# Kernel tuning notes

Hardware: AMD Instinct MI355X
Metric: run time of the kernel (lower is better)

## Reference

```python
import jax, jax.numpy as jnp
import numpy as np

B, H, S, D = 4, 16, 2048, 64

def setup_inputs() -> dict:
    key = jax.random.key(0)
    kq, kk, kv, km = jax.random.split(key, 4)
    q = jax.random.normal(kq, (B, H, S, D), dtype=jnp.float32)
    k = jax.random.normal(kk, (B, H, S, D), dtype=jnp.float32)
    v = jax.random.normal(kv, (B, H, S, D), dtype=jnp.float32)
    mask = jax.random.randint(km, (B, H, S, S), 0, 2, dtype=jnp.int32)
    return {"q": q, "k": k, "v": v, "mask": mask}

def reference(q, k, v, mask):
    d_k = q.shape[-1]
    scale = 1.0 / jnp.sqrt(jnp.asarray(d_k, dtype=q.dtype))
    # scores: [B, H, Sq, Sk]
    scores = jnp.einsum('bhqd,bhkd->bhqk', q, k) * scale
    scores = jnp.where(mask == 0, jnp.asarray(-10000.0, dtype=scores.dtype), scores)
    attn = jax.nn.softmax(scores, axis=-1)
    out = jnp.einsum('bhqk,bhkd->bhqd', attn, v)
    return (out, attn)
```

## Files before the change

### kernel.cpp

```cpp
#include <hip/hip_runtime.h>
#include <hip/hip_bf16.h>

typedef short bf16x8 __attribute__((ext_vector_type(8)));
typedef float f32x4 __attribute__((ext_vector_type(4)));
typedef unsigned short u16x8 __attribute__((ext_vector_type(8)));

#define DEVI static __device__ __forceinline__

constexpr int Bb = 4, Hh = 16, Ss = 2048, Dd = 64;
constexpr int BH = Bb * Hh;
constexpr float SCALE = 0.125f;
constexpr long QKV_ELEMS = (long)BH * Ss * Dd;
constexpr long MASK_ELEMS = (long)BH * Ss * Ss;

DEVI unsigned short f2bf(float f) {
  __hip_bfloat16 h = __float2bfloat16(f);
  unsigned short u;
  __builtin_memcpy(&u, &h, 2);
  return u;
}
DEVI float bflo(unsigned int u) { unsigned int x = u << 16;        float f; __builtin_memcpy(&f, &x, 4); return f; }
DEVI float bfhi(unsigned int u) { unsigned int x = u & 0xffff0000u; float f; __builtin_memcpy(&f, &x, 4); return f; }

DEVI int pidx(int q, int k) { return (q << 12) + ((k << 1) ^ ((q & 7) << 4)); }

DEVI bf16x8 cvt8(const float* p) {
  float4 a = *reinterpret_cast<const float4*>(p);
  float4 b = *reinterpret_cast<const float4*>(p + 4);
  bf16x8 r;
  r[0] = (short)f2bf(a.x); r[1] = (short)f2bf(a.y); r[2] = (short)f2bf(a.z); r[3] = (short)f2bf(a.w);
  r[4] = (short)f2bf(b.x); r[5] = (short)f2bf(b.y); r[6] = (short)f2bf(b.z); r[7] = (short)f2bf(b.w);
  return r;
}

__global__ __launch_bounds__(256) void bitpack(const int* __restrict__ mask,
                                               unsigned long long* __restrict__ bits)
{
  const long wid = (((long)blockIdx.x * 256 + threadIdx.x) >> 6);
  const int lane = threadIdx.x & 63;
  const long NW = ((long)gridDim.x * 256) >> 6;
  for (long W = wid; W < (MASK_ELEMS >> 8); W += NW) {
    const int* p = mask + (W << 8) + lane;
    const unsigned long long b0 = __ballot(__builtin_nontemporal_load(p) != 0);
    const unsigned long long b1 = __ballot(__builtin_nontemporal_load(p + 64) != 0);
    const unsigned long long b2 = __ballot(__builtin_nontemporal_load(p + 128) != 0);
    const unsigned long long b3 = __ballot(__builtin_nontemporal_load(p + 192) != 0);
    if (lane == 0) {
      ulonglong4 o; o.x = b0; o.y = b1; o.z = b2; o.w = b3;
      *reinterpret_cast<ulonglong4*>(bits + (W << 2)) = o;
    }
  }
}

__global__ __launch_bounds__(256) void cvt_qk(const float* __restrict__ q, const float* __restrict__ k,
                                              unsigned short* __restrict__ qb, unsigned short* __restrict__ kb)
{
  const long i = ((long)blockIdx.x * 256 + threadIdx.x) * 4;
  if (i >= QKV_ELEMS) return;
  const float4 a = *reinterpret_cast<const float4*>(q + i);
  ushort4 oa; oa.x = f2bf(a.x); oa.y = f2bf(a.y); oa.z = f2bf(a.z); oa.w = f2bf(a.w);
  *reinterpret_cast<ushort4*>(qb + i) = oa;
  const float4 b = *reinterpret_cast<const float4*>(k + i);
  ushort4 ob; ob.x = f2bf(b.x); ob.y = f2bf(b.y); ob.z = f2bf(b.z); ob.w = f2bf(b.w);
  *reinterpret_cast<ushort4*>(kb + i) = ob;
}

__global__ __launch_bounds__(256) void cvt_vt(const float* __restrict__ v, unsigned short* __restrict__ vt)
{
  __shared__ float tile[64][65];
  const int bh = blockIdx.x >> 5;
  const int s0 = (blockIdx.x & 31) << 6;
  const int t  = threadIdx.x;
  {
    const int c = (t & 15) << 2;
    const float* src = v + ((long)bh * Ss + s0) * Dd;
    for (int rr = (t >> 4); rr < 64; rr += 16) {
      const float4 a = *reinterpret_cast<const float4*>(src + rr * Dd + c);
      tile[rr][c] = a.x; tile[rr][c + 1] = a.y; tile[rr][c + 2] = a.z; tile[rr][c + 3] = a.w;
    }
  }
  __syncthreads();
  {
    const int d  = t >> 2;
    const int sc = (t & 3) << 4;
    unsigned short* dst = vt + ((long)bh * Dd + d) * Ss + s0 + sc;
    u16x8 v0, v1;
#pragma unroll
    for (int j = 0; j < 8; ++j) v0[j] = f2bf(tile[sc + j][d]);
#pragma unroll
    for (int j = 0; j < 8; ++j) v1[j] = f2bf(tile[sc + 8 + j][d]);
    *reinterpret_cast<u16x8*>(dst)     = v0;
    *reinterpret_cast<u16x8*>(dst + 8) = v1;
  }
}

template<bool PRE>
__global__ __launch_bounds__(256, 2)
void attn_main(const float* __restrict__ qf, const float* __restrict__ kf,
               const float* __restrict__ vf, const int* __restrict__ mask,
               const unsigned short* __restrict__ qb,
               const unsigned short* __restrict__ kbp,
               const unsigned short* __restrict__ vt,
               const unsigned long long* __restrict__ bits,
               float* __restrict__ out, float* __restrict__ attn)
{
  __shared__ __align__(16) char Pb[16 * 2048 * 2];
  __shared__ float rpart[4][16];
  __shared__ float rinv[16];

  const int tid  = threadIdx.x;
  const int wave = tid >> 6;
  const int lane = tid & 63;
  const int l15  = lane & 15;
  const int lg   = lane >> 4;

  const int bh    = blockIdx.x >> 7;
  const int qbase = (blockIdx.x & 127) << 4;

  bf16x8 qfrag0, qfrag1;
  {
    const long qrow = (long)(bh * Ss + qbase + l15) * Dd + lg * 8;
    if (PRE) {
      qfrag0 = *reinterpret_cast<const bf16x8*>(qb + qrow);
      qfrag1 = *reinterpret_cast<const bf16x8*>(qb + qrow + 32);
    } else {
      qfrag0 = cvt8(qf + qrow);
      qfrag1 = cvt8(qf + qrow + 32);
    }
  }

  float psum = 0.f;
  const long mrow = (long)(bh * Ss + qbase + l15) * Ss;

  for (int kt = 0; kt < Ss; kt += 64) {
    const int key0 = kt + (wave << 4);
    bf16x8 kfrag0, kfrag1;
    const long krow = (long)(bh * Ss + key0 + l15) * Dd + lg * 8;
    if (PRE) {
      kfrag0 = *reinterpret_cast<const bf16x8*>(kbp + krow);
      kfrag1 = *reinterpret_cast<const bf16x8*>(kbp + krow + 32);
    } else {
      kfrag0 = cvt8(kf + krow);
      kfrag1 = cvt8(kf + krow + 32);
    }
    const int k0 = key0 + (lg << 2);
    unsigned mm;
    if (PRE) {
      const unsigned long long e = (unsigned long long)(mrow + k0);
      const unsigned long long w = bits[e >> 6];
      mm = (unsigned)(w >> ((int)e & 63)) & 0xFu;
    } else {
      const int4 m4 = *reinterpret_cast<const int4*>(mask + mrow + k0);
      mm = (m4.x ? 1u : 0u) | (m4.y ? 2u : 0u) | (m4.z ? 4u : 0u) | (m4.w ? 8u : 0u);
    }
    f32x4 acc = {0.f, 0.f, 0.f, 0.f};
    acc = __builtin_amdgcn_mfma_f32_16x16x32_bf16(kfrag0, qfrag0, acc, 0, 0, 0);
    acc = __builtin_amdgcn_mfma_f32_16x16x32_bf16(kfrag1, qfrag1, acc, 0, 0, 0);
    const float p0 = (mm & 1u) ? __expf(acc[0] * SCALE) : 0.f;
    const float p1 = (mm & 2u) ? __expf(acc[1] * SCALE) : 0.f;
    const float p2 = (mm & 4u) ? __expf(acc[2] * SCALE) : 0.f;
    const float p3 = (mm & 8u) ? __expf(acc[3] * SCALE) : 0.f;
    psum += (p0 + p1) + (p2 + p3);
    uint2 w2;
    w2.x = (unsigned)f2bf(p0) | ((unsigned)f2bf(p1) << 16);
    w2.y = (unsigned)f2bf(p2) | ((unsigned)f2bf(p3) << 16);
    *reinterpret_cast<uint2*>(Pb + pidx(l15, k0)) = w2;
  }

  psum += __shfl_xor(psum, 16);
  psum += __shfl_xor(psum, 32);
  if (lane < 16) rpart[wave][l15] = psum;
  __syncthreads();
  if (tid < 16) {
    const float t = rpart[0][tid] + rpart[1][tid] + rpart[2][tid] + rpart[3][tid];
    rinv[tid] = (t > 0.f) ? (1.f / t) : 0.f;
  }
  __syncthreads();

  {
    const int r  = tid >> 4;
    const int cs = (tid & 15) << 3;
    const float inv = rinv[r];
    float* arow = attn + (long)(bh * Ss + qbase + r) * Ss;
#pragma unroll
    for (int it = 0; it < 16; ++it) {
      const int c0 = cs + (it << 7);
      const uint4 pk = *reinterpret_cast<const uint4*>(Pb + pidx(r, c0));
      f32x4 o0, o1;
      o0[0] = bflo(pk.x) * inv; o0[1] = bfhi(pk.x) * inv;
      o0[2] = bflo(pk.y) * inv; o0[3] = bfhi(pk.y) * inv;
      o1[0] = bflo(pk.z) * inv; o1[1] = bfhi(pk.z) * inv;
      o1[2] = bflo(pk.w) * inv; o1[3] = bfhi(pk.w) * inv;
      __builtin_nontemporal_store(o0, reinterpret_cast<f32x4*>(arow + c0));
      __builtin_nontemporal_store(o1, reinterpret_cast<f32x4*>(arow + c0 + 4));
    }
  }

  {
    const int dcol = (wave << 4) + l15;
    f32x4 oacc = {0.f, 0.f, 0.f, 0.f};
    const unsigned short* vrow = PRE ? (vt + (long)(bh * Dd + dcol) * Ss) : nullptr;
    const float* vcolf = PRE ? nullptr : (vf + (long)bh * Ss * Dd + dcol);
    for (int kk = 0; kk < Ss; kk += 32) {
      const int ka = kk + (lg << 3);
      const bf16x8 afrag = *reinterpret_cast<const bf16x8*>(Pb + pidx(l15, ka));
      bf16x8 bfrag;
      if (PRE) {
        bfrag = *reinterpret_cast<const bf16x8*>(vrow + ka);
      } else {
#pragma unroll
        for (int e = 0; e < 8; ++e) bfrag[e] = (short)f2bf(vcolf[(long)(ka + e) * Dd]);
      }
      oacc = __builtin_amdgcn_mfma_f32_16x16x32_bf16(afrag, bfrag, oacc, 0, 0, 0);
    }
    float* obase = out + (long)(bh * Ss + qbase) * Dd + dcol;
#pragma unroll
    for (int rg = 0; rg < 4; ++rg) {
      const int qrow = (lg << 2) + rg;
      __builtin_nontemporal_store(oacc[rg] * rinv[qrow], obase + qrow * Dd);
    }
  }
}

extern "C" void kernel_launch(void* const* d_in, const int* in_sizes, int n_in,
                              void* d_out, int out_size, void* d_ws, size_t ws_size,
                              hipStream_t stream)
{
  const float* q    = (const float*)d_in[0];
  const float* k    = (const float*)d_in[1];
  const float* v    = (const float*)d_in[2];
  const int*   mask = (const int*)d_in[3];
  float* out  = (float*)d_out;
  float* attn = out + QKV_ELEMS;

  const size_t bf16_bytes = (size_t)QKV_ELEMS * 2 * 3;
  const size_t bits_bytes = (size_t)(MASK_ELEMS >> 3);
  const size_t need = bf16_bytes + bits_bytes;
  if (ws_size >= need) {
    unsigned short* qb = (unsigned short*)d_ws;
    unsigned short* kb = qb + QKV_ELEMS;
    unsigned short* vt = kb + QKV_ELEMS;
    unsigned long long* bits = (unsigned long long*)((char*)d_ws + bf16_bytes);
    hipLaunchKernelGGL(bitpack, dim3(2048), dim3(256), 0, stream, mask, bits);
    hipLaunchKernelGGL(cvt_qk, dim3((unsigned)(QKV_ELEMS / 1024)), dim3(256), 0, stream, q, k, qb, kb);
    hipLaunchKernelGGL(cvt_vt, dim3(BH * 32), dim3(256), 0, stream, v, vt);
    hipLaunchKernelGGL((attn_main<true>), dim3(BH * 128), dim3(256), 0, stream,
                       q, k, v, mask, qb, kb, vt, bits, out, attn);
  } else {
    hipLaunchKernelGGL((attn_main<false>), dim3(BH * 128), dim3(256), 0, stream,
                       q, k, v, mask, nullptr, nullptr, nullptr, nullptr, out, attn);
  }
}
```

Before: 945.8 us.

## Recompute QK^T in a second pass to drop the 64KB P buffer and raise occupancy

Replaces the full 16x2048 bf16 probability buffer in shared memory with a two-pass scheme. The first pass computes QK^T only for the row sums, with each wave owning a contiguous 512-key range and caching its mask bits in registers. The second pass recomputes QK^T, normalizes, writes attn directly and feeds a small per-wave LDS staging tile into the PV MFMAs; per-wave partial outputs are then reduced through LDS. This cuts LDS use so four blocks can fit per CU (launch bounds 4), at the cost of doubling the QK MFMAs and K loads.

```diff
diff --git a/kernel.cpp b/kernel.cpp
--- a/kernel.cpp
+++ b/kernel.cpp
@@ -19,10 +19,6 @@
   __builtin_memcpy(&u, &h, 2);
   return u;
 }
-DEVI float bflo(unsigned int u) { unsigned int x = u << 16;        float f; __builtin_memcpy(&f, &x, 4); return f; }
-DEVI float bfhi(unsigned int u) { unsigned int x = u & 0xffff0000u; float f; __builtin_memcpy(&f, &x, 4); return f; }
-
-DEVI int pidx(int q, int k) { return (q << 12) + ((k << 1) ^ ((q & 7) << 4)); }
 
 DEVI bf16x8 cvt8(const float* p) {
   float4 a = *reinterpret_cast<const float4*>(p);
@@ -95,18 +91,19 @@
 }
 
 template<bool PRE>
-__global__ __launch_bounds__(256, 2)
+__global__ __launch_bounds__(256, 4)
 void attn_main(const float* __restrict__ qf, const float* __restrict__ kf,
                const float* __restrict__ vf, const int* __restrict__ mask,
                const unsigned short* __restrict__ qb,
                const unsigned short* __restrict__ kbp,
                const unsigned short* __restrict__ vt,
-               const unsigned long long* __restrict__ bits,
+               const unsigned* __restrict__ bits32,
                float* __restrict__ out, float* __restrict__ attn)
 {
-  __shared__ __align__(16) char Pb[16 * 2048 * 2];
+  __shared__ __align__(16) unsigned char Pv[4][1024];
+  __shared__ __align__(16) float Ored[4][16][64];
   __shared__ float rpart[4][16];
-  __shared__ float rinv[16];
+  __shared__ float rinv16[16];
 
   const int tid  = threadIdx.x;
   const int wave = tid >> 6;
@@ -116,55 +113,62 @@
 
   const int bh    = blockIdx.x >> 7;
   const int qbase = (blockIdx.x & 127) << 4;
-
-  bf16x8 qfrag0, qfrag1;
+  const int wbase = wave << 9;
+
+  bf16x8 qfr0, qfr1;
   {
     const long qrow = (long)(bh * Ss + qbase + l15) * Dd + lg * 8;
     if (PRE) {
-      qfrag0 = *reinterpret_cast<const bf16x8*>(qb + qrow);
-      qfrag1 = *reinterpret_cast<const bf16x8*>(qb + qrow + 32);
-    } else {
-      qfrag0 = cvt8(qf + qrow);
-      qfrag1 = cvt8(qf + qrow + 32);
-    }
-  }
-
+      qfr0 = *reinterpret_cast<const bf16x8*>(qb + qrow);
+      qfr1 = *reinterpret_cast<const bf16x8*>(qb + qrow + 32);
+    } else {
+      qfr0 = cvt8(qf + qrow);
+      qfr1 = cvt8(qf + qrow + 32);
+    }
+  }
+
+  const long mrowQ = (long)(bh * Ss + qbase + l15) * Ss;
+
+  unsigned mpack[4] = {0u, 0u, 0u, 0u};
   float psum = 0.f;
-  const long mrow = (long)(bh * Ss + qbase + l15) * Ss;
-
-  for (int kt = 0; kt < Ss; kt += 64) {
-    const int key0 = kt + (wave << 4);
-    bf16x8 kfrag0, kfrag1;
-    const long krow = (long)(bh * Ss + key0 + l15) * Dd + lg * 8;
-    if (PRE) {
-      kfrag0 = *reinterpret_cast<const bf16x8*>(kbp + krow);
-      kfrag1 = *reinterpret_cast<const bf16x8*>(kbp + krow + 32);
-    } else {
-      kfrag0 = cvt8(kf + krow);
-      kfrag1 = cvt8(kf + krow + 32);
-    }
-    const int k0 = key0 + (lg << 2);
+
+  for (int it = 0; it < 16; ++it) {
+    const int key0 = wbase + (it << 5);
+    const long kr0 = (long)(bh * Ss + key0 + l15) * Dd + lg * 8;
+    bf16x8 kA0, kA1, kB0, kB1;
+    if (PRE) {
+      kA0 = *reinterpret_cast<const bf16x8*>(kbp + kr0);
+      kA1 = *reinterpret_cast<const bf16x8*>(kbp + kr0 + 32);
+      kB0 = *reinterpret_cast<const bf16x8*>(kbp + kr0 + 16 * Dd);
+      kB1 = *reinterpret_cast<const bf16x8*>(kbp + kr0 + 16 * Dd + 32);
+    } else {
+      kA0 = cvt8(kf + kr0);        kA1 = cvt8(kf + kr0 + 32);
+      kB0 = cvt8(kf + kr0 + 16 * Dd); kB1 = cvt8(kf + kr0 + 16 * Dd + 32);
+    }
     unsigned mm;
     if (PRE) {
-      const unsigned long long e = (unsigned long long)(mrow + k0);
-      const unsigned long long w = bits[e >> 6];
-      mm = (unsigned)(w >> ((int)e & 63)) & 0xFu;
-    } else {
-      const int4 m4 = *reinterpret_cast<const int4*>(mask + mrow + k0);
-      mm = (m4.x ? 1u : 0u) | (m4.y ? 2u : 0u) | (m4.z ? 4u : 0u) | (m4.w ? 8u : 0u);
-    }
-    f32x4 acc = {0.f, 0.f, 0.f, 0.f};
-    acc = __builtin_amdgcn_mfma_f32_16x16x32_bf16(kfrag0, qfrag0, acc, 0, 0, 0);
-    acc = __builtin_amdgcn_mfma_f32_16x16x32_bf16(kfrag1, qfrag1, acc, 0, 0, 0);
-    const float p0 = (mm & 1u) ? __expf(acc[0] * SCALE) : 0.f;
-    const float p1 = (mm & 2u) ? __expf(acc[1] * SCALE) : 0.f;
-    const float p2 = (mm & 4u) ? __expf(acc[2] * SCALE) : 0.f;
-    const float p3 = (mm & 8u) ? __expf(acc[3] * SCALE) : 0.f;
-    psum += (p0 + p1) + (p2 + p3);
-    uint2 w2;
-    w2.x = (unsigned)f2bf(p0) | ((unsigned)f2bf(p1) << 16);
-    w2.y = (unsigned)f2bf(p2) | ((unsigned)f2bf(p3) << 16);
-    *reinterpret_cast<uint2*>(Pb + pidx(l15, k0)) = w2;
+      const unsigned w32 = bits32[(unsigned long long)(mrowQ + key0) >> 5];
+      mm = ((w32 >> (lg * 4)) & 0xFu) | (((w32 >> (16 + lg * 4)) & 0xFu) << 4);
+    } else {
+      const int4 m0 = *reinterpret_cast<const int4*>(mask + mrowQ + key0 + lg * 4);
+      const int4 m1 = *reinterpret_cast<const int4*>(mask + mrowQ + key0 + 16 + lg * 4);
+      mm = (m0.x ? 1u : 0u) | (m0.y ? 2u : 0u) | (m0.z ? 4u : 0u) | (m0.w ? 8u : 0u)
+         | (m1.x ? 16u : 0u) | (m1.y ? 32u : 0u) | (m1.z ? 64u : 0u) | (m1.w ? 128u : 0u);
+    }
+    mpack[it >> 2] |= mm << ((it & 3) << 3);
+    f32x4 aA = {0.f, 0.f, 0.f, 0.f}, aB = {0.f, 0.f, 0.f, 0.f};
+    aA = __builtin_amdgcn_mfma_f32_16x16x32_bf16(kA0, qfr0, aA, 0, 0, 0);
+    aA = __builtin_amdgcn_mfma_f32_16x16x32_bf16(kA1, qfr1, aA, 0, 0, 0);
+    aB = __builtin_amdgcn_mfma_f32_16x16x32_bf16(kB0, qfr0, aB, 0, 0, 0);
+    aB = __builtin_amdgcn_mfma_f32_16x16x32_bf16(kB1, qfr1, aB, 0, 0, 0);
+    psum += ((mm &   1u) ? __expf(aA[0] * SCALE) : 0.f)
+          + ((mm &   2u) ? __expf(aA[1] * SCALE) : 0.f)
+          + ((mm &   4u) ? __expf(aA[2] * SCALE) : 0.f)
+          + ((mm &   8u) ? __expf(aA[3] * SCALE) : 0.f)
+          + ((mm &  16u) ? __expf(aB[0] * SCALE) : 0.f)
+          + ((mm &  32u) ? __expf(aB[1] * SCALE) : 0.f)
+          + ((mm &  64u) ? __expf(aB[2] * SCALE) : 0.f)
+          + ((mm & 128u) ? __expf(aB[3] * SCALE) : 0.f);
   }
 
   psum += __shfl_xor(psum, 16);
@@ -173,52 +177,101 @@
   __syncthreads();
   if (tid < 16) {
     const float t = rpart[0][tid] + rpart[1][tid] + rpart[2][tid] + rpart[3][tid];
-    rinv[tid] = (t > 0.f) ? (1.f / t) : 0.f;
+    rinv16[tid] = (t > 0.f) ? (1.f / t) : 0.f;
   }
   __syncthreads();
-
+  const float inv = rinv16[l15];
+
+  unsigned char* myPv = &Pv[wave][0];
+  const int swz = (l15 & 3) << 4;
+  float* arow = attn + (long)(bh * Ss + qbase + l15) * Ss;
+  const unsigned short* vtb = PRE ? (vt + (long)(bh * Dd) * Ss) : nullptr;
+
+  f32x4 ob0 = {0.f,0.f,0.f,0.f}, ob1 = {0.f,0.f,0.f,0.f};
+  f32x4 ob2 = {0.f,0.f,0.f,0.f}, ob3 = {0.f,0.f,0.f,0.f};
+
+  for (int it = 0; it < 16; ++it) {
+    const int key0 = wbase + (it << 5);
+    const long kr0 = (long)(bh * Ss + key0 + l15) * Dd + lg * 8;
+    bf16x8 kA0, kA1, kB0, kB1;
+    if (PRE) {
+      kA0 = *reinterpret_cast<const bf16x8*>(kbp + kr0);
+      kA1 = *reinterpret_cast<const bf16x8*>(kbp + kr0 + 32);
+      kB0 = *reinterpret_cast<const bf16x8*>(kbp + kr0 + 16 * Dd);
+      kB1 = *reinterpret_cast<const bf16x8*>(kbp + kr0 + 16 * Dd + 32);
+    } else {
+      kA0 = cvt8(kf + kr0);        kA1 = cvt8(kf + kr0 + 32);
+      kB0 = cvt8(kf + kr0 + 16 * Dd); kB1 = cvt8(kf + kr0 + 16 * Dd + 32);
+    }
+    f32x4 aA = {0.f, 0.f, 0.f, 0.f}, aB = {0.f, 0.f, 0.f, 0.f};
+    aA = __builtin_amdgcn_mfma_f32_16x16x32_bf16(kA0, qfr0, aA, 0, 0, 0);
+    aA = __builtin_amdgcn_mfma_f32_16x16x32_bf16(kA1, qfr1, aA, 0, 0, 0);
+    aB = __builtin_amdgcn_mfma_f32_16x16x32_bf16(kB0, qfr0, aB, 0, 0, 0);
+    aB = __builtin_amdgcn_mfma_f32_16x16x32_bf16(kB1, qfr1, aB, 0, 0, 0);
+
+    const unsigned mm = (mpack[it >> 2] >> ((it & 3) << 3)) & 0xFFu;
+    const float p0 = (mm &   1u) ? __expf(aA[0] * SCALE) * inv : 0.f;
+    const float p1 = (mm &   2u) ? __expf(aA[1] * SCALE) * inv : 0.f;
+    const float p2 = (mm &   4u) ? __expf(aA[2] * SCALE) * inv : 0.f;
+    const float p3 = (mm &   8u) ? __expf(aA[3] * SCALE) * inv : 0.f;
+    const float p4 = (mm &  16u) ? __expf(aB[0] * SCALE) * inv : 0.f;
+    const float p5 = (mm &  32u) ? __expf(aB[1] * SCALE) * inv : 0.f;
+    const float p6 = (mm &  64u) ? __expf(aB[2] * SCALE) * inv : 0.f;
+    const float p7 = (mm & 128u) ? __expf(aB[3] * SCALE) * inv : 0.f;
+
+    f32x4 s0; s0[0] = p0; s0[1] = p1; s0[2] = p2; s0[3] = p3;
+    f32x4 s1; s1[0] = p4; s1[1] = p5; s1[2] = p6; s1[3] = p7;
+    __builtin_nontemporal_store(s0, reinterpret_cast<f32x4*>(arow + key0 + lg * 4));
+    __builtin_nontemporal_store(s1, reinterpret_cast<f32x4*>(arow + key0 + 16 + lg * 4));
+
+    uint2 w0, w1;
+    w0.x = (unsigned)f2bf(p0) | ((unsigned)f2bf(p1) << 16);
+    w0.y = (unsigned)f2bf(p2) | ((unsigned)f2bf(p3) << 16);
+    w1.x = (unsigned)f2bf(p4) | ((unsigned)f2bf(p5) << 16);
+    w1.y = (unsigned)f2bf(p6) | ((unsigned)f2bf(p7) << 16);
+    *reinterpret_cast<uint2*>(myPv + (l15 << 6) + (((lg << 3)      ) ^ swz)) = w0;
+    *reinterpret_cast<uint2*>(myPv + (l15 << 6) + ((32 + (lg << 3)) ^ swz)) = w1;
+
+    const bf16x8 af = *reinterpret_cast<const bf16x8*>(myPv + (l15 << 6) + (((lg << 4)) ^ swz));
+
+    if (PRE) {
+      const unsigned short* vp = vtb + key0 + lg * 8;
+      ob0 = __builtin_amdgcn_mfma_f32_16x16x32_bf16(af, *reinterpret_cast<const bf16x8*>(vp + (long)(l15)      * Ss), ob0, 0, 0, 0);
+      ob1 = __builtin_amdgcn_mfma_f32_16x16x32_bf16(af, *reinterpret_cast<const bf16x8*>(vp + (long)(16 + l15) * Ss), ob1, 0, 0, 0);
+      ob2 = __builtin_amdgcn_mfma_f32_16x16x32_bf16(af, *reinterpret_cast<const bf16x8*>(vp + (long)(32 + l15) * Ss), ob2, 0, 0, 0);
+      ob3 = __builtin_amdgcn_mfma_f32_16x16x32_bf16(af, *reinterpret_cast<const bf16x8*>(vp + (long)(48 + l15) * Ss), ob3, 0, 0, 0);
+    } else {
+      const float* vp = vf + (long)(bh * Ss + key0 + lg * 8) * Dd + l15;
+      bf16x8 b0, b1, b2, b3;
+#pragma unroll
+      for (int e = 0; e < 8; ++e) {
+        b0[e] = (short)f2bf(vp[e * Dd]);
+        b1[e] = (short)f2bf(vp[e * Dd + 16]);
+        b2[e] = (short)f2bf(vp[e * Dd + 32]);
+        b3[e] = (short)f2bf(vp[e * Dd + 48]);
+      }
+      ob0 = __builtin_amdgcn_mfma_f32_16x16x32_bf16(af, b0, ob0, 0, 0, 0);
+      ob1 = __builtin_amdgcn_mfma_f32_16x16x32_bf16(af, b1, ob1, 0, 0, 0);
+      ob2 = __builtin_amdgcn_mfma_f32_16x16x32_bf16(af, b2, ob2, 0, 0, 0);
+      ob3 = __builtin_amdgcn_mfma_f32_16x16x32_bf16(af, b3, ob3, 0, 0, 0);
+    }
+  }
+
+#pragma unroll
+  for (int r = 0; r < 4; ++r) {
+    Ored[wave][(lg << 2) + r][l15]      = ob0[r];
+    Ored[wave][(lg << 2) + r][16 + l15] = ob1[r];
+    Ored[wave][(lg << 2) + r][32 + l15] = ob2[r];
+    Ored[wave][(lg << 2) + r][48 + l15] = ob3[r];
+  }
+  __syncthreads();
   {
-    const int r  = tid >> 4;
-    const int cs = (tid & 15) << 3;
-    const float inv = rinv[r];
-    float* arow = attn + (long)(bh * Ss + qbase + r) * Ss;
-#pragma unroll
-    for (int it = 0; it < 16; ++it) {
-      const int c0 = cs + (it << 7);
-      const uint4 pk = *reinterpret_cast<const uint4*>(Pb + pidx(r, c0));
-      f32x4 o0, o1;
-      o0[0] = bflo(pk.x) * inv; o0[1] = bfhi(pk.x) * inv;
-      o0[2] = bflo(pk.y) * inv; o0[3] = bfhi(pk.y) * inv;
-      o1[0] = bflo(pk.z) * inv; o1[1] = bfhi(pk.z) * inv;
-      o1[2] = bflo(pk.w) * inv; o1[3] = bfhi(pk.w) * inv;
-      __builtin_nontemporal_store(o0, reinterpret_cast<f32x4*>(arow + c0));
-      __builtin_nontemporal_store(o1, reinterpret_cast<f32x4*>(arow + c0 + 4));
-    }
-  }
-
-  {
-    const int dcol = (wave << 4) + l15;
-    f32x4 oacc = {0.f, 0.f, 0.f, 0.f};
-    const unsigned short* vrow = PRE ? (vt + (long)(bh * Dd + dcol) * Ss) : nullptr;
-    const float* vcolf = PRE ? nullptr : (vf + (long)bh * Ss * Dd + dcol);
-    for (int kk = 0; kk < Ss; kk += 32) {
-      const int ka = kk + (lg << 3);
-      const bf16x8 afrag = *reinterpret_cast<const bf16x8*>(Pb + pidx(l15, ka));
-      bf16x8 bfrag;
-      if (PRE) {
-        bfrag = *reinterpret_cast<const bf16x8*>(vrow + ka);
-      } else {
-#pragma unroll
-        for (int e = 0; e < 8; ++e) bfrag[e] = (short)f2bf(vcolf[(long)(ka + e) * Dd]);
-      }
-      oacc = __builtin_amdgcn_mfma_f32_16x16x32_bf16(afrag, bfrag, oacc, 0, 0, 0);
-    }
-    float* obase = out + (long)(bh * Ss + qbase) * Dd + dcol;
-#pragma unroll
-    for (int rg = 0; rg < 4; ++rg) {
-      const int qrow = (lg << 2) + rg;
-      __builtin_nontemporal_store(oacc[rg] * rinv[qrow], obase + qrow * Dd);
-    }
+    const f32x4* Op = reinterpret_cast<const f32x4*>(&Ored[0][0][0]);
+    f32x4 t = Op[tid];
+    t += Op[256 + tid];
+    t += Op[512 + tid];
+    t += Op[768 + tid];
+    __builtin_nontemporal_store(t, reinterpret_cast<f32x4*>(out + (long)(bh * Ss + qbase) * Dd + (tid << 2)));
   }
 }
 
@@ -245,7 +298,7 @@
     hipLaunchKernelGGL(cvt_qk, dim3((unsigned)(QKV_ELEMS / 1024)), dim3(256), 0, stream, q, k, qb, kb);
     hipLaunchKernelGGL(cvt_vt, dim3(BH * 32), dim3(256), 0, stream, v, vt);
     hipLaunchKernelGGL((attn_main<true>), dim3(BH * 128), dim3(256), 0, stream,
-                       q, k, v, mask, qb, kb, vt, bits, out, attn);
+                       q, k, v, mask, qb, kb, vt, (const unsigned*)bits, out, attn);
   } else {
     hipLaunchKernelGGL((attn_main<false>), dim3(BH * 128), dim3(256), 0, stream,
                        q, k, v, mask, nullptr, nullptr, nullptr, nullptr, out, attn);
```

Result: slower. 1.026 ms (+8.4%).

## Halve query tile to 8 rows per block to raise occupancy

Applied to the files above, without the earlier changes.

Each block now handles 8 query rows instead of 16, so the shared-memory P buffer shrinks to 32 KB and the launch bound rises to 4 blocks per CU, with twice as many blocks launched. Each wave covers a contiguous 512-key range using two 16-key MFMAs per step, and the 16-row MFMA is half-used because rows are duplicated. The mask is read as 32-bit words, and the attn stores switch from nontemporal to ordinary stores. The output is reduced through shared memory before a vectorised store. The aim is better latency hiding and memory throughput, at the cost of duplicate MFMA work and reading K and V twice as often.

```diff
diff --git a/kernel.cpp b/kernel.cpp
--- a/kernel.cpp
+++ b/kernel.cpp
@@ -22,7 +22,7 @@
 DEVI float bflo(unsigned int u) { unsigned int x = u << 16;        float f; __builtin_memcpy(&f, &x, 4); return f; }
 DEVI float bfhi(unsigned int u) { unsigned int x = u & 0xffff0000u; float f; __builtin_memcpy(&f, &x, 4); return f; }
 
-DEVI int pidx(int q, int k) { return (q << 12) + ((k << 1) ^ ((q & 7) << 4)); }
+DEVI int p8(int r, int k) { return (r << 12) + ((k << 1) ^ (r << 4)); }
 
 DEVI bf16x8 cvt8(const float* p) {
   float4 a = *reinterpret_cast<const float4*>(p);
@@ -95,130 +95,151 @@
 }
 
 template<bool PRE>
-__global__ __launch_bounds__(256, 2)
+__global__ __launch_bounds__(256, 4)
 void attn_main(const float* __restrict__ qf, const float* __restrict__ kf,
                const float* __restrict__ vf, const int* __restrict__ mask,
                const unsigned short* __restrict__ qb,
                const unsigned short* __restrict__ kbp,
                const unsigned short* __restrict__ vt,
-               const unsigned long long* __restrict__ bits,
+               const unsigned* __restrict__ bits32,
                float* __restrict__ out, float* __restrict__ attn)
 {
-  __shared__ __align__(16) char Pb[16 * 2048 * 2];
-  __shared__ float rpart[4][16];
-  __shared__ float rinv[16];
+  __shared__ __align__(16) unsigned char Pb[8 * 4096];
+  __shared__ float rpart[4][8];
+  __shared__ float rinv8[8];
 
   const int tid  = threadIdx.x;
   const int wave = tid >> 6;
   const int lane = tid & 63;
   const int l15  = lane & 15;
   const int lg   = lane >> 4;
-
-  const int bh    = blockIdx.x >> 7;
-  const int qbase = (blockIdx.x & 127) << 4;
-
-  bf16x8 qfrag0, qfrag1;
-  {
-    const long qrow = (long)(bh * Ss + qbase + l15) * Dd + lg * 8;
+  const int r8   = l15 & 7;
+
+  const int bh    = blockIdx.x >> 8;
+  const int qbase = (blockIdx.x & 255) << 3;
+  const int wbase = wave << 9;
+
+  bf16x8 qfr0, qfr1;
+  {
+    const long qrow = (long)(bh * Ss + qbase + r8) * Dd + lg * 8;
     if (PRE) {
-      qfrag0 = *reinterpret_cast<const bf16x8*>(qb + qrow);
-      qfrag1 = *reinterpret_cast<const bf16x8*>(qb + qrow + 32);
+      qfr0 = *reinterpret_cast<const bf16x8*>(qb + qrow);
+      qfr1 = *reinterpret_cast<const bf16x8*>(qb + qrow + 32);
     } else {
-      qfrag0 = cvt8(qf + qrow);
-      qfrag1 = cvt8(qf + qrow + 32);
-    }
-  }
-
+      qfr0 = cvt8(qf + qrow);
+      qfr1 = cvt8(qf + qrow + 32);
+    }
+  }
+
+  const long mrowQ = (long)(bh * Ss + qbase + r8) * Ss;
   float psum = 0.f;
-  const long mrow = (long)(bh * Ss + qbase + l15) * Ss;
-
-  for (int kt = 0; kt < Ss; kt += 64) {
-    const int key0 = kt + (wave << 4);
-    bf16x8 kfrag0, kfrag1;
-    const long krow = (long)(bh * Ss + key0 + l15) * Dd + lg * 8;
+
+  for (int it = 0; it < 16; ++it) {
+    const int key0 = wbase + (it << 5);
+    const long kr0 = (long)(bh * Ss + key0 + l15) * Dd + lg * 8;
+    bf16x8 kA0, kA1, kB0, kB1;
     if (PRE) {
-      kfrag0 = *reinterpret_cast<const bf16x8*>(kbp + krow);
-      kfrag1 = *reinterpret_cast<const bf16x8*>(kbp + krow + 32);
+      kA0 = *reinterpret_cast<const bf16x8*>(kbp + kr0);
+      kA1 = *reinterpret_cast<const bf16x8*>(kbp + kr0 + 32);
+      kB0 = *reinterpret_cast<const bf16x8*>(kbp + kr0 + 16 * Dd);
+      kB1 = *reinterpret_cast<const bf16x8*>(kbp + kr0 + 16 * Dd + 32);
     } else {
-      kfrag0 = cvt8(kf + krow);
-      kfrag1 = cvt8(kf + krow + 32);
-    }
-    const int k0 = key0 + (lg << 2);
+      kA0 = cvt8(kf + kr0);           kA1 = cvt8(kf + kr0 + 32);
+      kB0 = cvt8(kf + kr0 + 16 * Dd); kB1 = cvt8(kf + kr0 + 16 * Dd + 32);
+    }
     unsigned mm;
     if (PRE) {
-      const unsigned long long e = (unsigned long long)(mrow + k0);
-      const unsigned long long w = bits[e >> 6];
-      mm = (unsigned)(w >> ((int)e & 63)) & 0xFu;
+      const unsigned w32 = bits32[(unsigned long long)(mrowQ + key0) >> 5];
+      mm = ((w32 >> (lg * 4)) & 0xFu) | (((w32 >> (16 + lg * 4)) & 0xFu) << 4);
     } else {
-      const int4 m4 = *reinterpret_cast<const int4*>(mask + mrow + k0);
-      mm = (m4.x ? 1u : 0u) | (m4.y ? 2u : 0u) | (m4.z ? 4u : 0u) | (m4.w ? 8u : 0u);
-    }
-    f32x4 acc = {0.f, 0.f, 0.f, 0.f};
-    acc = __builtin_amdgcn_mfma_f32_16x16x32_bf16(kfrag0, qfrag0, acc, 0, 0, 0);
-    acc = __builtin_amdgcn_mfma_f32_16x16x32_bf16(kfrag1, qfrag1, acc, 0, 0, 0);
-    const float p0 = (mm & 1u) ? __expf(acc[0] * SCALE) : 0.f;
-    const float p1 = (mm & 2u) ? __expf(acc[1] * SCALE) : 0.f;
-    const float p2 = (mm & 4u) ? __expf(acc[2] * SCALE) : 0.f;
-    const float p3 = (mm & 8u) ? __expf(acc[3] * SCALE) : 0.f;
-    psum += (p0 + p1) + (p2 + p3);
-    uint2 w2;
-    w2.x = (unsigned)f2bf(p0) | ((unsigned)f2bf(p1) << 16);
-    w2.y = (unsigned)f2bf(p2) | ((unsigned)f2bf(p3) << 16);
-    *reinterpret_cast<uint2*>(Pb + pidx(l15, k0)) = w2;
+      const int4 m0 = *reinterpret_cast<const int4*>(mask + mrowQ + key0 + lg * 4);
+      const int4 m1 = *reinterpret_cast<const int4*>(mask + mrowQ + key0 + 16 + lg * 4);
+      mm = (m0.x ? 1u : 0u) | (m0.y ? 2u : 0u) | (m0.z ? 4u : 0u) | (m0.w ? 8u : 0u)
+         | (m1.x ? 16u : 0u) | (m1.y ? 32u : 0u) | (m1.z ? 64u : 0u) | (m1.w ? 128u : 0u);
+    }
+    f32x4 aA = {0.f, 0.f, 0.f, 0.f}, aB = {0.f, 0.f, 0.f, 0.f};
+    aA = __builtin_amdgcn_mfma_f32_16x16x32_bf16(kA0, qfr0, aA, 0, 0, 0);
+    aA = __builtin_amdgcn_mfma_f32_16x16x32_bf16(kA1, qfr1, aA, 0, 0, 0);
+    aB = __builtin_amdgcn_mfma_f32_16x16x32_bf16(kB0, qfr0, aB, 0, 0, 0);
+    aB = __builtin_amdgcn_mfma_f32_16x16x32_bf16(kB1, qfr1, aB, 0, 0, 0);
+    const float p0 = (mm &   1u) ? __expf(aA[0] * SCALE) : 0.f;
+    const float p1 = (mm &   2u) ? __expf(aA[1] * SCALE) : 0.f;
+    const float p2 = (mm &   4u) ? __expf(aA[2] * SCALE) : 0.f;
+    const float p3 = (mm &   8u) ? __expf(aA[3] * SCALE) : 0.f;
+    const float p4 = (mm &  16u) ? __expf(aB[0] * SCALE) : 0.f;
+    const float p5 = (mm &  32u) ? __expf(aB[1] * SCALE) : 0.f;
+    const float p6 = (mm &  64u) ? __expf(aB[2] * SCALE) : 0.f;
+    const float p7 = (mm & 128u) ? __expf(aB[3] * SCALE) : 0.f;
+    psum += ((p0 + p1) + (p2 + p3)) + ((p4 + p5) + (p6 + p7));
+    uint2 w0, w1;
+    w0.x = (unsigned)f2bf(p0) | ((unsigned)f2bf(p1) << 16);
+    w0.y = (unsigned)f2bf(p2) | ((unsigned)f2bf(p3) << 16);
+    w1.x = (unsigned)f2bf(p4) | ((unsigned)f2bf(p5) << 16);
+    w1.y = (unsigned)f2bf(p6) | ((unsigned)f2bf(p7) << 16);
+    const int  addr = (l15 < 8) ? p8(r8, key0 + lg * 4) : p8(r8, key0 + 16 + lg * 4);
+    const uint2 wv  = (l15 < 8) ? w0 : w1;
+    *reinterpret_cast<uint2*>(Pb + addr) = wv;
   }
 
   psum += __shfl_xor(psum, 16);
   psum += __shfl_xor(psum, 32);
-  if (lane < 16) rpart[wave][l15] = psum;
-  __syncthreads();
-  if (tid < 16) {
+  if (lane < 8) rpart[wave][lane] = psum;
+  __syncthreads();
+  if (tid < 8) {
     const float t = rpart[0][tid] + rpart[1][tid] + rpart[2][tid] + rpart[3][tid];
-    rinv[tid] = (t > 0.f) ? (1.f / t) : 0.f;
-  }
-  __syncthreads();
-
-  {
-    const int r  = tid >> 4;
-    const int cs = (tid & 15) << 3;
-    const float inv = rinv[r];
+    rinv8[tid] = (t > 0.f) ? (1.f / t) : 0.f;
+  }
+  __syncthreads();
+
+  {
+    const int r  = (wave << 1) + (lane >> 5);
+    const int cb = (lane & 31) << 3;
+    const float inv = rinv8[r];
     float* arow = attn + (long)(bh * Ss + qbase + r) * Ss;
 #pragma unroll
-    for (int it = 0; it < 16; ++it) {
-      const int c0 = cs + (it << 7);
-      const uint4 pk = *reinterpret_cast<const uint4*>(Pb + pidx(r, c0));
+    for (int ch = 0; ch < 8; ++ch) {
+      const int c0 = cb + (ch << 8);
+      const uint4 pk = *reinterpret_cast<const uint4*>(Pb + p8(r, c0));
       f32x4 o0, o1;
       o0[0] = bflo(pk.x) * inv; o0[1] = bfhi(pk.x) * inv;
       o0[2] = bflo(pk.y) * inv; o0[3] = bfhi(pk.y) * inv;
       o1[0] = bflo(pk.z) * inv; o1[1] = bfhi(pk.z) * inv;
       o1[2] = bflo(pk.w) * inv; o1[3] = bfhi(pk.w) * inv;
-      __builtin_nontemporal_store(o0, reinterpret_cast<f32x4*>(arow + c0));
-      __builtin_nontemporal_store(o1, reinterpret_cast<f32x4*>(arow + c0 + 4));
-    }
-  }
-
-  {
-    const int dcol = (wave << 4) + l15;
-    f32x4 oacc = {0.f, 0.f, 0.f, 0.f};
+      *reinterpret_cast<f32x4*>(arow + c0)     = o0;
+      *reinterpret_cast<f32x4*>(arow + c0 + 4) = o1;
+    }
+  }
+
+  f32x4 oacc = {0.f, 0.f, 0.f, 0.f};
+  const int dcol = (wave << 4) + l15;
+  {
     const unsigned short* vrow = PRE ? (vt + (long)(bh * Dd + dcol) * Ss) : nullptr;
     const float* vcolf = PRE ? nullptr : (vf + (long)bh * Ss * Dd + dcol);
     for (int kk = 0; kk < Ss; kk += 32) {
       const int ka = kk + (lg << 3);
-      const bf16x8 afrag = *reinterpret_cast<const bf16x8*>(Pb + pidx(l15, ka));
-      bf16x8 bfrag;
+      const bf16x8 af = *reinterpret_cast<const bf16x8*>(Pb + p8(r8, ka));
+      bf16x8 bfr;
       if (PRE) {
-        bfrag = *reinterpret_cast<const bf16x8*>(vrow + ka);
+        bfr = *reinterpret_cast<const bf16x8*>(vrow + ka);
       } else {
 #pragma unroll
-        for (int e = 0; e < 8; ++e) bfrag[e] = (short)f2bf(vcolf[(long)(ka + e) * Dd]);
+        for (int e = 0; e < 8; ++e) bfr[e] = (short)f2bf(vcolf[(long)(ka + e) * Dd]);
       }
-      oacc = __builtin_amdgcn_mfma_f32_16x16x32_bf16(afrag, bfrag, oacc, 0, 0, 0);
-    }
-    float* obase = out + (long)(bh * Ss + qbase) * Dd + dcol;
-#pragma unroll
-    for (int rg = 0; rg < 4; ++rg) {
-      const int qrow = (lg << 2) + rg;
-      __builtin_nontemporal_store(oacc[rg] * rinv[qrow], obase + qrow * Dd);
-    }
+      oacc = __builtin_amdgcn_mfma_f32_16x16x32_bf16(af, bfr, oacc, 0, 0, 0);
+    }
+  }
+  __syncthreads();
+  float* OredF = reinterpret_cast<float*>(Pb);
+  if (lg < 2) {
+#pragma unroll
+    for (int r = 0; r < 4; ++r)
+      OredF[((lg << 2) + r) * 64 + dcol] = oacc[r];
+  }
+  __syncthreads();
+  if (tid < 128) {
+    f32x4 t = reinterpret_cast<const f32x4*>(Pb)[tid];
+    t *= rinv8[tid >> 4];
+    *reinterpret_cast<f32x4*>(out + (long)(bh * Ss + qbase) * Dd + (tid << 2)) = t;
   }
 }
 
@@ -244,10 +265,10 @@
     hipLaunchKernelGGL(bitpack, dim3(2048), dim3(256), 0, stream, mask, bits);
     hipLaunchKernelGGL(cvt_qk, dim3((unsigned)(QKV_ELEMS / 1024)), dim3(256), 0, stream, q, k, qb, kb);
     hipLaunchKernelGGL(cvt_vt, dim3(BH * 32), dim3(256), 0, stream, v, vt);
-    hipLaunchKernelGGL((attn_main<true>), dim3(BH * 128), dim3(256), 0, stream,
-                       q, k, v, mask, qb, kb, vt, bits, out, attn);
+    hipLaunchKernelGGL((attn_main<true>), dim3(BH * 256), dim3(256), 0, stream,
+                       q, k, v, mask, qb, kb, vt, (const unsigned*)bits, out, attn);
   } else {
-    hipLaunchKernelGGL((attn_main<false>), dim3(BH * 128), dim3(256), 0, stream,
+    hipLaunchKernelGGL((attn_main<false>), dim3(BH * 256), dim3(256), 0, stream,
                        q, k, v, mask, nullptr, nullptr, nullptr, nullptr, out, attn);
   }
 }
```

New measurement: 1.327 ms. 1.4x slower.
